# Kernel tuning notes

Measured on AMD Instinct MI355X. Metric: run time of the kernel, lower is better.

The kernel has to match this reference:

```python
import jax, jax.numpy as jnp
import numpy as np
import math

WIN = 7
PAD = WIN // 2
DOWN = 4
OCC_SCALE = 2.0
GROUPS = 8
GN_EPS = 1e-5
OCC_EPS = 1e-6


def group_norm(x, w, b):
    # x: [B, C, H, W]; normalize within channel groups (torch GroupNorm)
    B, C, H, W = x.shape
    xg = x.reshape(B, GROUPS, C // GROUPS, H, W)
    mu = xg.mean(axis=(2, 3, 4), keepdims=True)
    var = xg.var(axis=(2, 3, 4), keepdims=True)
    xn = ((xg - mu) * jax.lax.rsqrt(var + GN_EPS)).reshape(B, C, H, W)
    return xn * w[None, :, None, None] + b[None, :, None, None]


def avg_pool(x):
    s = jax.lax.reduce_window(x, 0.0, jax.lax.add, (1, 1, DOWN, DOWN), (1, 1, DOWN, DOWN), 'VALID')
    return s / (DOWN * DOWN)


def max_pool(x):
    return jax.lax.reduce_window(x, -jnp.inf, jax.lax.max, (1, 1, DOWN, DOWN), (1, 1, DOWN, DOWN), 'VALID')


def unfold(x):
    # kernel positions in row-major (i-major) order, matching torch layout.
    B, C, h, w = x.shape
    xp = jnp.pad(x, ((0, 0), (0, 0), (PAD, PAD), (PAD, PAD)))
    pats = jnp.stack([xp[:, :, i:i + h, j:j + w] for i in range(WIN) for j in range(WIN)], axis=2)
    return pats


def reference(img_bev, rad_bev, occ_prob, Wq, Wk, Wv, Wo, gq_w, gq_b, gk_w, gk_b, alpha):
    B, C, H, W = img_bev.shape
    img = avg_pool(img_bev)
    rad = max_pool(rad_bev)
    occ = max_pool(occ_prob)

    q = group_norm(jnp.einsum('oc,bchw->bohw', Wq, img), gq_w, gq_b)
    k = group_norm(jnp.einsum('oc,bchw->bohw', Wk, rad), gk_w, gk_b)
    v = jnp.einsum('oc,bchw->bohw', Wv, rad)

    _, d, h, w = q.shape
    HW = h * w
    P = WIN * WIN

    k_nb = unfold(k).reshape(B, d, P, HW).transpose(0, 3, 2, 1)  # [B,HW,P,d]
    v_nb = unfold(v).reshape(B, d, P, HW).transpose(0, 3, 2, 1)  # [B,HW,P,d]
    q_flat = q.reshape(B, d, HW).transpose(0, 2, 1)              # [B,HW,d]

    logits = jnp.einsum('bnd,bnpd->bnp', q_flat, k_nb) / math.sqrt(d)
    occ_nb = unfold(occ).reshape(B, P, HW).transpose(0, 2, 1)    # [B,HW,P]
    logits = logits + OCC_SCALE * jnp.log(jnp.clip(occ_nb, OCC_EPS, None))

    att = jax.nn.softmax(logits, axis=-1)
    msg = jnp.einsum('bnp,bnpd->bnd', att, v_nb)                 # [B,HW,d]
    msg = msg.transpose(0, 2, 1).reshape(B, d, h, w)
    msg = jnp.einsum('od,bdhw->bohw', Wo, msg)
    msg = msg * jnp.clip(occ, 0.0, 1.0)
    msg = jax.image.resize(msg, (B, C, H, W), method='bilinear')  # align_corners=False
    return img_bev + alpha * msg


def setup_inputs() -> dict:
    key = jax.random.key(0)
    ks = jax.random.split(key, 12)
    B, C_IMG, C_RAD, H, W, D = 2, 256, 128, 384, 384, 64
    inp = {
        'img_bev': jax.random.normal(ks[0], (B, C_IMG, H, W), jnp.float32),
        'rad_bev': jax.random.normal(ks[1], (B, C_RAD, H, W), jnp.float32),
        'occ_prob': jax.random.uniform(ks[2], (B, 1, H, W), jnp.float32),
        'Wq': jax.random.normal(ks[3], (D, C_IMG), jnp.float32) / np.sqrt(C_IMG),
        'Wk': jax.random.normal(ks[4], (D, C_RAD), jnp.float32) / np.sqrt(C_RAD),
        'Wv': jax.random.normal(ks[5], (D, C_RAD), jnp.float32) / np.sqrt(C_RAD),
        'Wo': jax.random.normal(ks[6], (C_IMG, D), jnp.float32) / np.sqrt(D),
        'gq_w': jnp.ones((D,), jnp.float32),
        'gq_b': jnp.zeros((D,), jnp.float32),
        'gk_w': jnp.ones((D,), jnp.float32),
        'gk_b': jnp.zeros((D,), jnp.float32),
        'alpha': jnp.float32(0.1),
    }
    return inp
```

## Files before the change

### kernel.cpp

```cpp
#include <hip/hip_runtime.h>
#include <math.h>


namespace {
constexpr int HIN  = 384;
constexpr int WIN_ = 384;
constexpr int HP   = 96;
constexpr int WPX  = 96;
constexpr int NP   = HP * WPX;
constexpr int CIMG = 256;
constexpr int CRAD = 128;
constexpr int DD   = 64;
constexpr int BB   = 2;
constexpr float OOB_LOGIT = -27.631021115928547f;

constexpr size_t OFF_IMGP = 0;
constexpr size_t OFF_RADP = OFF_IMGP + (size_t)BB * CIMG * NP;
constexpr size_t OFF_OCCP = OFF_RADP + (size_t)BB * CRAD * NP;
constexpr size_t OFF_OCCL = OFF_OCCP + (size_t)BB * NP;
constexpr size_t OFF_Q    = OFF_OCCL + (size_t)BB * NP;
constexpr size_t OFF_K    = OFF_Q + (size_t)BB * NP * DD;
constexpr size_t OFF_V    = OFF_K + (size_t)BB * NP * DD;
constexpr size_t OFF_MSG  = OFF_V + (size_t)BB * NP * DD;
constexpr size_t OFF_MSGO = OFF_MSG + (size_t)BB * NP * DD;
constexpr size_t OFF_WOT  = OFF_MSGO + (size_t)BB * CIMG * NP;
constexpr size_t OFF_STAT = OFF_WOT + (size_t)DD * CIMG;
constexpr size_t OFF_COEF = OFF_STAT + 64;
}

__global__ __launch_bounds__(256) void pool_kernel(const float* __restrict__ img,
                                                   const float* __restrict__ rad,
                                                   const float* __restrict__ occ,
                                                   float* __restrict__ ws) {
  int bid = blockIdx.x;
  int tid = threadIdx.x;
  const float* src;
  float* dst;
  float* occl = nullptr;
  int mode;
  if (bid < BB * CIMG) {
    src = img + (size_t)bid * HIN * WIN_;
    dst = ws + OFF_IMGP + (size_t)bid * NP;
    mode = 0;
  } else if (bid < BB * CIMG + BB * CRAD) {
    int r = bid - BB * CIMG;
    src = rad + (size_t)r * HIN * WIN_;
    dst = ws + OFF_RADP + (size_t)r * NP;
    mode = 1;
  } else {
    int r = bid - BB * CIMG - BB * CRAD;
    src = occ + (size_t)r * HIN * WIN_;
    dst = ws + OFF_OCCP + (size_t)r * NP;
    occl = ws + OFF_OCCL + (size_t)r * NP;
    mode = 2;
  }
  for (int it = 0; it < NP / 256; ++it) {
    int idx = it * 256 + tid;
    int oy = idx / WPX, ox = idx % WPX;
    const float* p = src + (size_t)(oy * 4) * WIN_ + ox * 4;
    if (mode == 0) {
      float s = 0.f;
#pragma unroll
      for (int r = 0; r < 4; ++r) {
        float4 v = *(const float4*)(p + (size_t)r * WIN_);
        s += v.x + v.y + v.z + v.w;
      }
      dst[idx] = s * 0.0625f;
    } else {
      float m = -INFINITY;
#pragma unroll
      for (int r = 0; r < 4; ++r) {
        float4 v = *(const float4*)(p + (size_t)r * WIN_);
        m = fmaxf(m, fmaxf(fmaxf(v.x, v.y), fmaxf(v.z, v.w)));
      }
      dst[idx] = m;
      if (mode == 2) occl[idx] = 2.0f * logf(fmaxf(m, 1e-6f));
    }
  }
}

__global__ __launch_bounds__(256) void proj_q_kernel(const float* __restrict__ Wq,
                                                     float* __restrict__ ws) {
  __shared__ float Xs[32 * 64];
  __shared__ float Wss[32 * 64];
  __shared__ float sstat[16];
  int bid = blockIdx.x;
  int b = bid / (NP / 64);
  int n0 = (bid % (NP / 64)) * 64;
  int tid = threadIdx.x;
  int og = tid & 15, ng = tid >> 4;
  if (tid < 16) sstat[tid] = 0.f;
  float4 acc[4];
#pragma unroll
  for (int j = 0; j < 4; ++j) acc[j] = make_float4(0.f, 0.f, 0.f, 0.f);
  const float* X = ws + OFF_IMGP + (size_t)b * CIMG * NP;
  for (int c0 = 0; c0 < CIMG; c0 += 32) {
    {
      int cc = tid >> 3, seg = tid & 7;
      const float* g = X + (size_t)(c0 + cc) * NP + n0 + seg * 8;
      float4 a0 = *(const float4*)g;
      float4 a1 = *(const float4*)(g + 4);
      *(float4*)&Xs[cc * 64 + seg * 8] = a0;
      *(float4*)&Xs[cc * 64 + seg * 8 + 4] = a1;
    }
    {
      int o = tid & 63, q8 = tid >> 6;
      const float* g = Wq + (size_t)o * CIMG + c0 + q8 * 8;
      float4 a0 = *(const float4*)g;
      float4 a1 = *(const float4*)(g + 4);
      Wss[(q8 * 8 + 0) * 64 + o] = a0.x;
      Wss[(q8 * 8 + 1) * 64 + o] = a0.y;
      Wss[(q8 * 8 + 2) * 64 + o] = a0.z;
      Wss[(q8 * 8 + 3) * 64 + o] = a0.w;
      Wss[(q8 * 8 + 4) * 64 + o] = a1.x;
      Wss[(q8 * 8 + 5) * 64 + o] = a1.y;
      Wss[(q8 * 8 + 6) * 64 + o] = a1.z;
      Wss[(q8 * 8 + 7) * 64 + o] = a1.w;
    }
    __syncthreads();
#pragma unroll
    for (int cc = 0; cc < 32; ++cc) {
      float4 wv = *(const float4*)&Wss[cc * 64 + og * 4];
      float4 xv = *(const float4*)&Xs[cc * 64 + ng * 4];
      acc[0].x = fmaf(wv.x, xv.x, acc[0].x); acc[0].y = fmaf(wv.y, xv.x, acc[0].y);
      acc[0].z = fmaf(wv.z, xv.x, acc[0].z); acc[0].w = fmaf(wv.w, xv.x, acc[0].w);
      acc[1].x = fmaf(wv.x, xv.y, acc[1].x); acc[1].y = fmaf(wv.y, xv.y, acc[1].y);
      acc[1].z = fmaf(wv.z, xv.y, acc[1].z); acc[1].w = fmaf(wv.w, xv.y, acc[1].w);
      acc[2].x = fmaf(wv.x, xv.z, acc[2].x); acc[2].y = fmaf(wv.y, xv.z, acc[2].y);
      acc[2].z = fmaf(wv.z, xv.z, acc[2].z); acc[2].w = fmaf(wv.w, xv.z, acc[2].w);
      acc[3].x = fmaf(wv.x, xv.w, acc[3].x); acc[3].y = fmaf(wv.y, xv.w, acc[3].y);
      acc[3].z = fmaf(wv.z, xv.w, acc[3].z); acc[3].w = fmaf(wv.w, xv.w, acc[3].w);
    }
    __syncthreads();
  }
  float* outq = ws + OFF_Q + (size_t)b * NP * DD;
#pragma unroll
  for (int j = 0; j < 4; ++j) {
    *(float4*)&outq[(size_t)(n0 + ng * 4 + j) * DD + og * 4] = acc[j];
  }
  float s1 = 0.f, s2 = 0.f;
#pragma unroll
  for (int j = 0; j < 4; ++j) {
    s1 += acc[j].x + acc[j].y + acc[j].z + acc[j].w;
    s2 += acc[j].x * acc[j].x + acc[j].y * acc[j].y + acc[j].z * acc[j].z + acc[j].w * acc[j].w;
  }
  int g = og >> 1;
  atomicAdd(&sstat[g * 2], s1);
  atomicAdd(&sstat[g * 2 + 1], s2);
  __syncthreads();
  if (tid < 16) atomicAdd(&ws[OFF_STAT + b * 16 + tid], sstat[tid]);
}

__global__ __launch_bounds__(256) void proj_kv_kernel(const float* __restrict__ Wk,
                                                      const float* __restrict__ Wv,
                                                      float* __restrict__ ws) {
  __shared__ float Xs[32 * 64];
  __shared__ float Wsk[32 * 64];
  __shared__ float Wsv[32 * 64];
  __shared__ float sstat[16];
  int bid = blockIdx.x;
  int b = bid / (NP / 64);
  int n0 = (bid % (NP / 64)) * 64;
  int tid = threadIdx.x;
  int og = tid & 15, ng = tid >> 4;
  if (tid < 16) sstat[tid] = 0.f;
  float4 acck[4], accv[4];
#pragma unroll
  for (int j = 0; j < 4; ++j) {
    acck[j] = make_float4(0.f, 0.f, 0.f, 0.f);
    accv[j] = make_float4(0.f, 0.f, 0.f, 0.f);
  }
  const float* X = ws + OFF_RADP + (size_t)b * CRAD * NP;
  for (int c0 = 0; c0 < CRAD; c0 += 32) {
    {
      int cc = tid >> 3, seg = tid & 7;
      const float* g = X + (size_t)(c0 + cc) * NP + n0 + seg * 8;
      float4 a0 = *(const float4*)g;
      float4 a1 = *(const float4*)(g + 4);
      *(float4*)&Xs[cc * 64 + seg * 8] = a0;
      *(float4*)&Xs[cc * 64 + seg * 8 + 4] = a1;
    }
    {
      int o = tid & 63, q8 = tid >> 6;
      const float* gk = Wk + (size_t)o * CRAD + c0 + q8 * 8;
      const float* gv = Wv + (size_t)o * CRAD + c0 + q8 * 8;
      float4 k0 = *(const float4*)gk;
      float4 k1 = *(const float4*)(gk + 4);
      float4 v0 = *(const float4*)gv;
      float4 v1 = *(const float4*)(gv + 4);
      Wsk[(q8 * 8 + 0) * 64 + o] = k0.x; Wsk[(q8 * 8 + 1) * 64 + o] = k0.y;
      Wsk[(q8 * 8 + 2) * 64 + o] = k0.z; Wsk[(q8 * 8 + 3) * 64 + o] = k0.w;
      Wsk[(q8 * 8 + 4) * 64 + o] = k1.x; Wsk[(q8 * 8 + 5) * 64 + o] = k1.y;
      Wsk[(q8 * 8 + 6) * 64 + o] = k1.z; Wsk[(q8 * 8 + 7) * 64 + o] = k1.w;
      Wsv[(q8 * 8 + 0) * 64 + o] = v0.x; Wsv[(q8 * 8 + 1) * 64 + o] = v0.y;
      Wsv[(q8 * 8 + 2) * 64 + o] = v0.z; Wsv[(q8 * 8 + 3) * 64 + o] = v0.w;
      Wsv[(q8 * 8 + 4) * 64 + o] = v1.x; Wsv[(q8 * 8 + 5) * 64 + o] = v1.y;
      Wsv[(q8 * 8 + 6) * 64 + o] = v1.z; Wsv[(q8 * 8 + 7) * 64 + o] = v1.w;
    }
    __syncthreads();
#pragma unroll
    for (int cc = 0; cc < 32; ++cc) {
      float4 wk = *(const float4*)&Wsk[cc * 64 + og * 4];
      float4 wv = *(const float4*)&Wsv[cc * 64 + og * 4];
      float4 xv = *(const float4*)&Xs[cc * 64 + ng * 4];
      float xs;
      xs = xv.x;
      acck[0].x = fmaf(wk.x, xs, acck[0].x); acck[0].y = fmaf(wk.y, xs, acck[0].y);
      acck[0].z = fmaf(wk.z, xs, acck[0].z); acck[0].w = fmaf(wk.w, xs, acck[0].w);
      accv[0].x = fmaf(wv.x, xs, accv[0].x); accv[0].y = fmaf(wv.y, xs, accv[0].y);
      accv[0].z = fmaf(wv.z, xs, accv[0].z); accv[0].w = fmaf(wv.w, xs, accv[0].w);
      xs = xv.y;
      acck[1].x = fmaf(wk.x, xs, acck[1].x); acck[1].y = fmaf(wk.y, xs, acck[1].y);
      acck[1].z = fmaf(wk.z, xs, acck[1].z); acck[1].w = fmaf(wk.w, xs, acck[1].w);
      accv[1].x = fmaf(wv.x, xs, accv[1].x); accv[1].y = fmaf(wv.y, xs, accv[1].y);
      accv[1].z = fmaf(wv.z, xs, accv[1].z); accv[1].w = fmaf(wv.w, xs, accv[1].w);
      xs = xv.z;
      acck[2].x = fmaf(wk.x, xs, acck[2].x); acck[2].y = fmaf(wk.y, xs, acck[2].y);
      acck[2].z = fmaf(wk.z, xs, acck[2].z); acck[2].w = fmaf(wk.w, xs, acck[2].w);
      accv[2].x = fmaf(wv.x, xs, accv[2].x); accv[2].y = fmaf(wv.y, xs, accv[2].y);
      accv[2].z = fmaf(wv.z, xs, accv[2].z); accv[2].w = fmaf(wv.w, xs, accv[2].w);
      xs = xv.w;
      acck[3].x = fmaf(wk.x, xs, acck[3].x); acck[3].y = fmaf(wk.y, xs, acck[3].y);
      acck[3].z = fmaf(wk.z, xs, acck[3].z); acck[3].w = fmaf(wk.w, xs, acck[3].w);
      accv[3].x = fmaf(wv.x, xs, accv[3].x); accv[3].y = fmaf(wv.y, xs, accv[3].y);
      accv[3].z = fmaf(wv.z, xs, accv[3].z); accv[3].w = fmaf(wv.w, xs, accv[3].w);
    }
    __syncthreads();
  }
  float* outk = ws + OFF_K + (size_t)b * NP * DD;
  float* outv = ws + OFF_V + (size_t)b * NP * DD;
#pragma unroll
  for (int j = 0; j < 4; ++j) {
    *(float4*)&outk[(size_t)(n0 + ng * 4 + j) * DD + og * 4] = acck[j];
    *(float4*)&outv[(size_t)(n0 + ng * 4 + j) * DD + og * 4] = accv[j];
  }
  float s1 = 0.f, s2 = 0.f;
#pragma unroll
  for (int j = 0; j < 4; ++j) {
    s1 += acck[j].x + acck[j].y + acck[j].z + acck[j].w;
    s2 += acck[j].x * acck[j].x + acck[j].y * acck[j].y + acck[j].z * acck[j].z +
          acck[j].w * acck[j].w;
  }
  int g = og >> 1;
  atomicAdd(&sstat[g * 2], s1);
  atomicAdd(&sstat[g * 2 + 1], s2);
  __syncthreads();
  if (tid < 16) atomicAdd(&ws[OFF_STAT + 32 + b * 16 + tid], sstat[tid]);
}

__global__ void coef_kernel(const float* __restrict__ gqw, const float* __restrict__ gqb,
                            const float* __restrict__ gkw, const float* __restrict__ gkb,
                            const float* __restrict__ Wo, float* __restrict__ ws) {
  int tid = threadIdx.x;
  const float Nf = 8.f * NP;
  float* stat = ws + OFF_STAT;
  float* coef = ws + OFF_COEF;
  if (tid < 128) {
    int b = tid >> 6, o = tid & 63, g = o >> 3;
    float s1 = stat[(b * 8 + g) * 2], s2 = stat[(b * 8 + g) * 2 + 1];
    float mu = s1 / Nf;
    float var = s2 / Nf - mu * mu;
    float rstd = rsqrtf(var + 1e-5f);
    coef[tid] = rstd * gqw[o];
    coef[128 + tid] = gqb[o] - mu * rstd * gqw[o];
    s1 = stat[32 + (b * 8 + g) * 2];
    s2 = stat[32 + (b * 8 + g) * 2 + 1];
    mu = s1 / Nf;
    var = s2 / Nf - mu * mu;
    rstd = rsqrtf(var + 1e-5f);
    coef[256 + tid] = rstd * gkw[o];
    coef[384 + tid] = gkb[o] - mu * rstd * gkw[o];
  }
  float* WoT = ws + OFF_WOT;
  for (int i = 0; i < 64; ++i) WoT[i * 256 + tid] = Wo[(size_t)tid * 64 + i];
}

__global__ __launch_bounds__(256) void attn_kernel(float* __restrict__ ws) {
  int tid = threadIdx.x;
  int lane = tid & 63, widx = tid >> 6;
  int pos = blockIdx.x * 4 + widx;
  int b = pos / NP, n = pos % NP;
  int y = n / WPX, x = n % WPX;
  const float* coef = ws + OFF_COEF;
  float aq = coef[b * 64 + lane], bq = coef[128 + b * 64 + lane];
  float ak = coef[256 + b * 64 + lane], bk = coef[384 + b * 64 + lane];
  const float* qb = ws + OFF_Q + (size_t)b * NP * DD;
  const float* kb = ws + OFF_K + (size_t)b * NP * DD;
  const float* vb = ws + OFF_V + (size_t)b * NP * DD;
  const float* occl = ws + OFF_OCCL + (size_t)b * NP;
  float qn = fmaf(qb[(size_t)n * DD + lane], aq, bq);
  float m = -1e30f, l = 0.f, acc = 0.f;
  for (int dy = -3; dy <= 3; ++dy) {
    int yy = y + dy;
    for (int dx = -3; dx <= 3; ++dx) {
      int xx = x + dx;
      bool in = ((unsigned)yy < (unsigned)HP) && ((unsigned)xx < (unsigned)WPX);
      float logit, vv;
      if (in) {
        int nb = yy * WPX + xx;
        float kn = fmaf(kb[(size_t)nb * DD + lane], ak, bk);
        float t = qn * kn;
        t += __shfl_xor(t, 1);
        t += __shfl_xor(t, 2);
        t += __shfl_xor(t, 4);
        t += __shfl_xor(t, 8);
        t += __shfl_xor(t, 16);
        t += __shfl_xor(t, 32);
        logit = fmaf(t, 0.125f, occl[nb]);
        vv = vb[(size_t)nb * DD + lane];
      } else {
        logit = OOB_LOGIT;
        vv = 0.f;
      }
      float mn = fmaxf(m, logit);
      float cor = __expf(m - mn);
      float wgt = __expf(logit - mn);
      l = fmaf(l, cor, wgt);
      acc = fmaf(acc, cor, wgt * vv);
      m = mn;
    }
  }
  ws[OFF_MSG + ((size_t)b * NP + n) * DD + lane] = acc / l;
}

__global__ __launch_bounds__(256) void wo_kernel(float* __restrict__ ws) {
  __shared__ float Ms[32 * 64];
  __shared__ float T[256 * 33];
  int bid = blockIdx.x;
  int b = bid / (NP / 32);
  int n0 = (bid % (NP / 32)) * 32;
  int tid = threadIdx.x;
  const float* msg = ws + OFF_MSG + ((size_t)b * NP + n0) * DD;
  {
    float4 a0 = *(const float4*)(msg + tid * 8);
    float4 a1 = *(const float4*)(msg + tid * 8 + 4);
    *(float4*)&Ms[tid * 8] = a0;
    *(float4*)&Ms[tid * 8 + 4] = a1;
  }
  __syncthreads();
  const float* WoT = ws + OFF_WOT;
  float acc[32];
#pragma unroll
  for (int n = 0; n < 32; ++n) acc[n] = 0.f;
  for (int dc = 0; dc < 64; dc += 16) {
    float w[16];
#pragma unroll
    for (int i = 0; i < 16; ++i) w[i] = WoT[(size_t)(dc + i) * 256 + tid];
#pragma unroll
    for (int n = 0; n < 32; ++n) {
      const float* mr = &Ms[n * 64 + dc];
      float s = acc[n];
#pragma unroll
      for (int i = 0; i < 16; ++i) s = fmaf(w[i], mr[i], s);
      acc[n] = s;
    }
  }
  const float* occp = ws + OFF_OCCP + (size_t)b * NP + n0;
#pragma unroll
  for (int n = 0; n < 32; ++n) {
    float oc = occp[n];
    oc = fminf(fmaxf(oc, 0.f), 1.f);
    T[tid * 33 + n] = acc[n] * oc;
  }
  __syncthreads();
  float* msgo = ws + OFF_MSGO + (size_t)b * CIMG * NP;
  for (int rep = 0; rep < 32; ++rep) {
    int idx = rep * 256 + tid;
    int c = idx >> 5, n = idx & 31;
    msgo[(size_t)c * NP + n0 + n] = T[c * 33 + n];
  }
}

__global__ __launch_bounds__(256) void final_kernel(const float* __restrict__ img,
                                                    const float* __restrict__ ws,
                                                    const float* __restrict__ alpha_p,
                                                    float* __restrict__ out) {
  size_t idx = (size_t)blockIdx.x * 256 + threadIdx.x;
  int xq = (int)(idx % 96);
  size_t t1 = idx / 96;
  int y = (int)(t1 % 384);
  size_t t2 = t1 / 384;
  int c = (int)(t2 % 256);
  int b = (int)(t2 / 256);
  float alpha = *alpha_p;
  const float* mrow = ws + OFF_MSGO + (size_t)(b * 256 + c) * NP;
  float sy = y * 0.25f - 0.375f;
  float jf = floorf(sy);
  float fy = sy - jf;
  int j0 = (int)jf;
  int j1 = j0 + 1;
  j0 = max(j0, 0);
  j1 = min(j1, HP - 1);
  int iL = max(xq - 1, 0), iC = xq, iR = min(xq + 1, WPX - 1);
  const float* r0 = mrow + (size_t)j0 * WPX;
  const float* r1 = mrow + (size_t)j1 * WPX;
  float cL = fmaf(fy, r1[iL] - r0[iL], r0[iL]);
  float cC = fmaf(fy, r1[iC] - r0[iC], r0[iC]);
  float cR = fmaf(fy, r1[iR] - r0[iR], r0[iR]);
  float4 v;
  v.x = fmaf(0.625f, cC - cL, cL);
  v.y = fmaf(0.875f, cC - cL, cL);
  v.z = fmaf(0.125f, cR - cC, cC);
  v.w = fmaf(0.375f, cR - cC, cC);
  size_t base = ((size_t)(b * 256 + c) * 384 + y) * 384 + (size_t)xq * 4;
  float4 im = *(const float4*)(img + base);
  float4 o;
  o.x = fmaf(alpha, v.x, im.x);
  o.y = fmaf(alpha, v.y, im.y);
  o.z = fmaf(alpha, v.z, im.z);
  o.w = fmaf(alpha, v.w, im.w);
  *(float4*)(out + base) = o;
}

extern "C" void kernel_launch(void* const* d_in, const int* in_sizes, int n_in,
                              void* d_out, int out_size, void* d_ws, size_t ws_size,
                              hipStream_t stream) {
  const float* img = (const float*)d_in[0];
  const float* rad = (const float*)d_in[1];
  const float* occ = (const float*)d_in[2];
  const float* Wq = (const float*)d_in[3];
  const float* Wk = (const float*)d_in[4];
  const float* Wv = (const float*)d_in[5];
  const float* Wo = (const float*)d_in[6];
  const float* gqw = (const float*)d_in[7];
  const float* gqb = (const float*)d_in[8];
  const float* gkw = (const float*)d_in[9];
  const float* gkb = (const float*)d_in[10];
  const float* alpha = (const float*)d_in[11];
  float* ws = (float*)d_ws;
  float* out = (float*)d_out;

  hipMemsetAsync(ws + OFF_STAT, 0, 64 * sizeof(float), stream);
  pool_kernel<<<BB * CIMG + BB * CRAD + BB, 256, 0, stream>>>(img, rad, occ, ws);
  proj_q_kernel<<<BB * (NP / 64), 256, 0, stream>>>(Wq, ws);
  proj_kv_kernel<<<BB * (NP / 64), 256, 0, stream>>>(Wk, Wv, ws);
  coef_kernel<<<1, 256, 0, stream>>>(gqw, gqb, gkw, gkb, Wo, ws);
  attn_kernel<<<BB * NP / 4, 256, 0, stream>>>(ws);
  wo_kernel<<<BB * (NP / 32), 256, 0, stream>>>(ws);
  final_kernel<<<(BB * 256 * 384 * 96) / 256, 256, 0, stream>>>(img, ws, alpha, out);
}
```

Measured before the change: 822.6 us.

## Merge Q and KV projection launches; pack four query positions per wavefront in attention

The two projection kernels are combined into one launch, with blocks split by index between the Q path and the K/V path. This lets both sets of work share the GPU at once and removes one launch boundary. The attention kernel now handles four query positions per 64-lane wavefront, with each lane owning four channels via float4 loads. That cuts the dot-product shuffle reduction from six steps to four and quarters the per-position exp/softmax bookkeeping. The cost is more registers per lane and a 16-lane reduction instead of a full-wave one.

```diff
diff --git a/kernel.cpp b/kernel.cpp
--- a/kernel.cpp
+++ b/kernel.cpp
@@ -79,173 +79,171 @@
   }
 }
 
-__global__ __launch_bounds__(256) void proj_q_kernel(const float* __restrict__ Wq,
-                                                     float* __restrict__ ws) {
-  __shared__ float Xs[32 * 64];
-  __shared__ float Wss[32 * 64];
-  __shared__ float sstat[16];
+__global__ __launch_bounds__(256) void proj_kernel(const float* __restrict__ Wq,
+                                                   const float* __restrict__ Wk,
+                                                   const float* __restrict__ Wv,
+                                                   float* __restrict__ ws) {
+  __shared__ float smem[3 * 32 * 64 + 16];
+  float* Xs = smem;
+  float* Wa = smem + 2048;
+  float* Wb = smem + 4096;
+  float* sstat = smem + 6144;
   int bid = blockIdx.x;
-  int b = bid / (NP / 64);
-  int n0 = (bid % (NP / 64)) * 64;
   int tid = threadIdx.x;
   int og = tid & 15, ng = tid >> 4;
   if (tid < 16) sstat[tid] = 0.f;
-  float4 acc[4];
-#pragma unroll
-  for (int j = 0; j < 4; ++j) acc[j] = make_float4(0.f, 0.f, 0.f, 0.f);
-  const float* X = ws + OFF_IMGP + (size_t)b * CIMG * NP;
-  for (int c0 = 0; c0 < CIMG; c0 += 32) {
-    {
-      int cc = tid >> 3, seg = tid & 7;
-      const float* g = X + (size_t)(c0 + cc) * NP + n0 + seg * 8;
-      float4 a0 = *(const float4*)g;
-      float4 a1 = *(const float4*)(g + 4);
-      *(float4*)&Xs[cc * 64 + seg * 8] = a0;
-      *(float4*)&Xs[cc * 64 + seg * 8 + 4] = a1;
-    }
-    {
-      int o = tid & 63, q8 = tid >> 6;
-      const float* g = Wq + (size_t)o * CIMG + c0 + q8 * 8;
-      float4 a0 = *(const float4*)g;
-      float4 a1 = *(const float4*)(g + 4);
-      Wss[(q8 * 8 + 0) * 64 + o] = a0.x;
-      Wss[(q8 * 8 + 1) * 64 + o] = a0.y;
-      Wss[(q8 * 8 + 2) * 64 + o] = a0.z;
-      Wss[(q8 * 8 + 3) * 64 + o] = a0.w;
-      Wss[(q8 * 8 + 4) * 64 + o] = a1.x;
-      Wss[(q8 * 8 + 5) * 64 + o] = a1.y;
-      Wss[(q8 * 8 + 6) * 64 + o] = a1.z;
-      Wss[(q8 * 8 + 7) * 64 + o] = a1.w;
-    }
+  const int NBLK = BB * (NP / 64);
+
+  if (bid < NBLK) {
+    int b = bid / (NP / 64);
+    int n0 = (bid % (NP / 64)) * 64;
+    float4 acc[4];
+#pragma unroll
+    for (int j = 0; j < 4; ++j) acc[j] = make_float4(0.f, 0.f, 0.f, 0.f);
+    const float* X = ws + OFF_IMGP + (size_t)b * CIMG * NP;
+    for (int c0 = 0; c0 < CIMG; c0 += 32) {
+      {
+        int cc = tid >> 3, seg = tid & 7;
+        const float* g = X + (size_t)(c0 + cc) * NP + n0 + seg * 8;
+        float4 a0 = *(const float4*)g;
+        float4 a1 = *(const float4*)(g + 4);
+        *(float4*)&Xs[cc * 64 + seg * 8] = a0;
+        *(float4*)&Xs[cc * 64 + seg * 8 + 4] = a1;
+      }
+      {
+        int o = tid & 63, q8 = tid >> 6;
+        const float* g = Wq + (size_t)o * CIMG + c0 + q8 * 8;
+        float4 a0 = *(const float4*)g;
+        float4 a1 = *(const float4*)(g + 4);
+        Wa[(q8 * 8 + 0) * 64 + o] = a0.x;
+        Wa[(q8 * 8 + 1) * 64 + o] = a0.y;
+        Wa[(q8 * 8 + 2) * 64 + o] = a0.z;
+        Wa[(q8 * 8 + 3) * 64 + o] = a0.w;
+        Wa[(q8 * 8 + 4) * 64 + o] = a1.x;
+        Wa[(q8 * 8 + 5) * 64 + o] = a1.y;
+        Wa[(q8 * 8 + 6) * 64 + o] = a1.z;
+        Wa[(q8 * 8 + 7) * 64 + o] = a1.w;
+      }
+      __syncthreads();
+#pragma unroll
+      for (int cc = 0; cc < 32; ++cc) {
+        float4 wv = *(const float4*)&Wa[cc * 64 + og * 4];
+        float4 xv = *(const float4*)&Xs[cc * 64 + ng * 4];
+        acc[0].x = fmaf(wv.x, xv.x, acc[0].x); acc[0].y = fmaf(wv.y, xv.x, acc[0].y);
+        acc[0].z = fmaf(wv.z, xv.x, acc[0].z); acc[0].w = fmaf(wv.w, xv.x, acc[0].w);
+        acc[1].x = fmaf(wv.x, xv.y, acc[1].x); acc[1].y = fmaf(wv.y, xv.y, acc[1].y);
+        acc[1].z = fmaf(wv.z, xv.y, acc[1].z); acc[1].w = fmaf(wv.w, xv.y, acc[1].w);
+        acc[2].x = fmaf(wv.x, xv.z, acc[2].x); acc[2].y = fmaf(wv.y, xv.z, acc[2].y);
+        acc[2].z = fmaf(wv.z, xv.z, acc[2].z); acc[2].w = fmaf(wv.w, xv.z, acc[2].w);
+        acc[3].x = fmaf(wv.x, xv.w, acc[3].x); acc[3].y = fmaf(wv.y, xv.w, acc[3].y);
+        acc[3].z = fmaf(wv.z, xv.w, acc[3].z); acc[3].w = fmaf(wv.w, xv.w, acc[3].w);
+      }
+      __syncthreads();
+    }
+    float* outq = ws + OFF_Q + (size_t)b * NP * DD;
+#pragma unroll
+    for (int j = 0; j < 4; ++j) {
+      *(float4*)&outq[(size_t)(n0 + ng * 4 + j) * DD + og * 4] = acc[j];
+    }
+    float s1 = 0.f, s2 = 0.f;
+#pragma unroll
+    for (int j = 0; j < 4; ++j) {
+      s1 += acc[j].x + acc[j].y + acc[j].z + acc[j].w;
+      s2 += acc[j].x * acc[j].x + acc[j].y * acc[j].y + acc[j].z * acc[j].z +
+            acc[j].w * acc[j].w;
+    }
+    int g = og >> 1;
+    atomicAdd(&sstat[g * 2], s1);
+    atomicAdd(&sstat[g * 2 + 1], s2);
     __syncthreads();
-#pragma unroll
-    for (int cc = 0; cc < 32; ++cc) {
-      float4 wv = *(const float4*)&Wss[cc * 64 + og * 4];
-      float4 xv = *(const float4*)&Xs[cc * 64 + ng * 4];
-      acc[0].x = fmaf(wv.x, xv.x, acc[0].x); acc[0].y = fmaf(wv.y, xv.x, acc[0].y);
-      acc[0].z = fmaf(wv.z, xv.x, acc[0].z); acc[0].w = fmaf(wv.w, xv.x, acc[0].w);
-      acc[1].x = fmaf(wv.x, xv.y, acc[1].x); acc[1].y = fmaf(wv.y, xv.y, acc[1].y);
-      acc[1].z = fmaf(wv.z, xv.y, acc[1].z); acc[1].w = fmaf(wv.w, xv.y, acc[1].w);
-      acc[2].x = fmaf(wv.x, xv.z, acc[2].x); acc[2].y = fmaf(wv.y, xv.z, acc[2].y);
-      acc[2].z = fmaf(wv.z, xv.z, acc[2].z); acc[2].w = fmaf(wv.w, xv.z, acc[2].w);
-      acc[3].x = fmaf(wv.x, xv.w, acc[3].x); acc[3].y = fmaf(wv.y, xv.w, acc[3].y);
-      acc[3].z = fmaf(wv.z, xv.w, acc[3].z); acc[3].w = fmaf(wv.w, xv.w, acc[3].w);
-    }
+    if (tid < 16) atomicAdd(&ws[OFF_STAT + b * 16 + tid], sstat[tid]);
+  } else {
+    int r = bid - NBLK;
+    int b = r / (NP / 64);
+    int n0 = (r % (NP / 64)) * 64;
+    float4 acck[4], accv[4];
+#pragma unroll
+    for (int j = 0; j < 4; ++j) {
+      acck[j] = make_float4(0.f, 0.f, 0.f, 0.f);
+      accv[j] = make_float4(0.f, 0.f, 0.f, 0.f);
+    }
+    const float* X = ws + OFF_RADP + (size_t)b * CRAD * NP;
+    for (int c0 = 0; c0 < CRAD; c0 += 32) {
+      {
+        int cc = tid >> 3, seg = tid & 7;
+        const float* g = X + (size_t)(c0 + cc) * NP + n0 + seg * 8;
+        float4 a0 = *(const float4*)g;
+        float4 a1 = *(const float4*)(g + 4);
+        *(float4*)&Xs[cc * 64 + seg * 8] = a0;
+        *(float4*)&Xs[cc * 64 + seg * 8 + 4] = a1;
+      }
+      {
+        int o = tid & 63, q8 = tid >> 6;
+        const float* gk = Wk + (size_t)o * CRAD + c0 + q8 * 8;
+        const float* gv = Wv + (size_t)o * CRAD + c0 + q8 * 8;
+        float4 k0 = *(const float4*)gk;
+        float4 k1 = *(const float4*)(gk + 4);
+        float4 v0 = *(const float4*)gv;
+        float4 v1 = *(const float4*)(gv + 4);
+        Wa[(q8 * 8 + 0) * 64 + o] = k0.x; Wa[(q8 * 8 + 1) * 64 + o] = k0.y;
+        Wa[(q8 * 8 + 2) * 64 + o] = k0.z; Wa[(q8 * 8 + 3) * 64 + o] = k0.w;
+        Wa[(q8 * 8 + 4) * 64 + o] = k1.x; Wa[(q8 * 8 + 5) * 64 + o] = k1.y;
+        Wa[(q8 * 8 + 6) * 64 + o] = k1.z; Wa[(q8 * 8 + 7) * 64 + o] = k1.w;
+        Wb[(q8 * 8 + 0) * 64 + o] = v0.x; Wb[(q8 * 8 + 1) * 64 + o] = v0.y;
+        Wb[(q8 * 8 + 2) * 64 + o] = v0.z; Wb[(q8 * 8 + 3) * 64 + o] = v0.w;
+        Wb[(q8 * 8 + 4) * 64 + o] = v1.x; Wb[(q8 * 8 + 5) * 64 + o] = v1.y;
+        Wb[(q8 * 8 + 6) * 64 + o] = v1.z; Wb[(q8 * 8 + 7) * 64 + o] = v1.w;
+      }
+      __syncthreads();
+#pragma unroll
+      for (int cc = 0; cc < 32; ++cc) {
+        float4 wk = *(const float4*)&Wa[cc * 64 + og * 4];
+        float4 wv = *(const float4*)&Wb[cc * 64 + og * 4];
+        float4 xv = *(const float4*)&Xs[cc * 64 + ng * 4];
+        float xs;
+        xs = xv.x;
+        acck[0].x = fmaf(wk.x, xs, acck[0].x); acck[0].y = fmaf(wk.y, xs, acck[0].y);
+        acck[0].z = fmaf(wk.z, xs, acck[0].z); acck[0].w = fmaf(wk.w, xs, acck[0].w);
+        accv[0].x = fmaf(wv.x, xs, accv[0].x); accv[0].y = fmaf(wv.y, xs, accv[0].y);
+        accv[0].z = fmaf(wv.z, xs, accv[0].z); accv[0].w = fmaf(wv.w, xs, accv[0].w);
+        xs = xv.y;
+        acck[1].x = fmaf(wk.x, xs, acck[1].x); acck[1].y = fmaf(wk.y, xs, acck[1].y);
+        acck[1].z = fmaf(wk.z, xs, acck[1].z); acck[1].w = fmaf(wk.w, xs, acck[1].w);
+        accv[1].x = fmaf(wv.x, xs, accv[1].x); accv[1].y = fmaf(wv.y, xs, accv[1].y);
+        accv[1].z = fmaf(wv.z, xs, accv[1].z); accv[1].w = fmaf(wv.w, xs, accv[1].w);
+        xs = xv.z;
+        acck[2].x = fmaf(wk.x, xs, acck[2].x); acck[2].y = fmaf(wk.y, xs, acck[2].y);
+        acck[2].z = fmaf(wk.z, xs, acck[2].z); acck[2].w = fmaf(wk.w, xs, acck[2].w);
+        accv[2].x = fmaf(wv.x, xs, accv[2].x); accv[2].y = fmaf(wv.y, xs, accv[2].y);
+        accv[2].z = fmaf(wv.z, xs, accv[2].z); accv[2].w = fmaf(wv.w, xs, accv[2].w);
+        xs = xv.w;
+        acck[3].x = fmaf(wk.x, xs, acck[3].x); acck[3].y = fmaf(wk.y, xs, acck[3].y);
+        acck[3].z = fmaf(wk.z, xs, acck[3].z); acck[3].w = fmaf(wk.w, xs, acck[3].w);
+        accv[3].x = fmaf(wv.x, xs, accv[3].x); accv[3].y = fmaf(wv.y, xs, accv[3].y);
+        accv[3].z = fmaf(wv.z, xs, accv[3].z); accv[3].w = fmaf(wv.w, xs, accv[3].w);
+      }
+      __syncthreads();
+    }
+    float* outk = ws + OFF_K + (size_t)b * NP * DD;
+    float* outv = ws + OFF_V + (size_t)b * NP * DD;
+#pragma unroll
+    for (int j = 0; j < 4; ++j) {
+      *(float4*)&outk[(size_t)(n0 + ng * 4 + j) * DD + og * 4] = acck[j];
+      *(float4*)&outv[(size_t)(n0 + ng * 4 + j) * DD + og * 4] = accv[j];
+    }
+    float s1 = 0.f, s2 = 0.f;
+#pragma unroll
+    for (int j = 0; j < 4; ++j) {
+      s1 += acck[j].x + acck[j].y + acck[j].z + acck[j].w;
+      s2 += acck[j].x * acck[j].x + acck[j].y * acck[j].y + acck[j].z * acck[j].z +
+            acck[j].w * acck[j].w;
+    }
+    int g = og >> 1;
+    atomicAdd(&sstat[g * 2], s1);
+    atomicAdd(&sstat[g * 2 + 1], s2);
     __syncthreads();
-  }
-  float* outq = ws + OFF_Q + (size_t)b * NP * DD;
-#pragma unroll
-  for (int j = 0; j < 4; ++j) {
-    *(float4*)&outq[(size_t)(n0 + ng * 4 + j) * DD + og * 4] = acc[j];
-  }
-  float s1 = 0.f, s2 = 0.f;
-#pragma unroll
-  for (int j = 0; j < 4; ++j) {
-    s1 += acc[j].x + acc[j].y + acc[j].z + acc[j].w;
-    s2 += acc[j].x * acc[j].x + acc[j].y * acc[j].y + acc[j].z * acc[j].z + acc[j].w * acc[j].w;
-  }
-  int g = og >> 1;
-  atomicAdd(&sstat[g * 2], s1);
-  atomicAdd(&sstat[g * 2 + 1], s2);
-  __syncthreads();
-  if (tid < 16) atomicAdd(&ws[OFF_STAT + b * 16 + tid], sstat[tid]);
-}
-
-__global__ __launch_bounds__(256) void proj_kv_kernel(const float* __restrict__ Wk,
-                                                      const float* __restrict__ Wv,
-                                                      float* __restrict__ ws) {
-  __shared__ float Xs[32 * 64];
-  __shared__ float Wsk[32 * 64];
-  __shared__ float Wsv[32 * 64];
-  __shared__ float sstat[16];
-  int bid = blockIdx.x;
-  int b = bid / (NP / 64);
-  int n0 = (bid % (NP / 64)) * 64;
-  int tid = threadIdx.x;
-  int og = tid & 15, ng = tid >> 4;
-  if (tid < 16) sstat[tid] = 0.f;
-  float4 acck[4], accv[4];
-#pragma unroll
-  for (int j = 0; j < 4; ++j) {
-    acck[j] = make_float4(0.f, 0.f, 0.f, 0.f);
-    accv[j] = make_float4(0.f, 0.f, 0.f, 0.f);
-  }
-  const float* X = ws + OFF_RADP + (size_t)b * CRAD * NP;
-  for (int c0 = 0; c0 < CRAD; c0 += 32) {
-    {
-      int cc = tid >> 3, seg = tid & 7;
-      const float* g = X + (size_t)(c0 + cc) * NP + n0 + seg * 8;
-      float4 a0 = *(const float4*)g;
-      float4 a1 = *(const float4*)(g + 4);
-      *(float4*)&Xs[cc * 64 + seg * 8] = a0;
-      *(float4*)&Xs[cc * 64 + seg * 8 + 4] = a1;
-    }
-    {
-      int o = tid & 63, q8 = tid >> 6;
-      const float* gk = Wk + (size_t)o * CRAD + c0 + q8 * 8;
-      const float* gv = Wv + (size_t)o * CRAD + c0 + q8 * 8;
-      float4 k0 = *(const float4*)gk;
-      float4 k1 = *(const float4*)(gk + 4);
-      float4 v0 = *(const float4*)gv;
-      float4 v1 = *(const float4*)(gv + 4);
-      Wsk[(q8 * 8 + 0) * 64 + o] = k0.x; Wsk[(q8 * 8 + 1) * 64 + o] = k0.y;
-      Wsk[(q8 * 8 + 2) * 64 + o] = k0.z; Wsk[(q8 * 8 + 3) * 64 + o] = k0.w;
-      Wsk[(q8 * 8 + 4) * 64 + o] = k1.x; Wsk[(q8 * 8 + 5) * 64 + o] = k1.y;
-      Wsk[(q8 * 8 + 6) * 64 + o] = k1.z; Wsk[(q8 * 8 + 7) * 64 + o] = k1.w;
-      Wsv[(q8 * 8 + 0) * 64 + o] = v0.x; Wsv[(q8 * 8 + 1) * 64 + o] = v0.y;
-      Wsv[(q8 * 8 + 2) * 64 + o] = v0.z; Wsv[(q8 * 8 + 3) * 64 + o] = v0.w;
-      Wsv[(q8 * 8 + 4) * 64 + o] = v1.x; Wsv[(q8 * 8 + 5) * 64 + o] = v1.y;
-      Wsv[(q8 * 8 + 6) * 64 + o] = v1.z; Wsv[(q8 * 8 + 7) * 64 + o] = v1.w;
-    }
-    __syncthreads();
-#pragma unroll
-    for (int cc = 0; cc < 32; ++cc) {
-      float4 wk = *(const float4*)&Wsk[cc * 64 + og * 4];
-      float4 wv = *(const float4*)&Wsv[cc * 64 + og * 4];
-      float4 xv = *(const float4*)&Xs[cc * 64 + ng * 4];
-      float xs;
-      xs = xv.x;
-      acck[0].x = fmaf(wk.x, xs, acck[0].x); acck[0].y = fmaf(wk.y, xs, acck[0].y);
-      acck[0].z = fmaf(wk.z, xs, acck[0].z); acck[0].w = fmaf(wk.w, xs, acck[0].w);
-      accv[0].x = fmaf(wv.x, xs, accv[0].x); accv[0].y = fmaf(wv.y, xs, accv[0].y);
-      accv[0].z = fmaf(wv.z, xs, accv[0].z); accv[0].w = fmaf(wv.w, xs, accv[0].w);
-      xs = xv.y;
-      acck[1].x = fmaf(wk.x, xs, acck[1].x); acck[1].y = fmaf(wk.y, xs, acck[1].y);
-      acck[1].z = fmaf(wk.z, xs, acck[1].z); acck[1].w = fmaf(wk.w, xs, acck[1].w);
-      accv[1].x = fmaf(wv.x, xs, accv[1].x); accv[1].y = fmaf(wv.y, xs, accv[1].y);
-      accv[1].z = fmaf(wv.z, xs, accv[1].z); accv[1].w = fmaf(wv.w, xs, accv[1].w);
-      xs = xv.z;
-      acck[2].x = fmaf(wk.x, xs, acck[2].x); acck[2].y = fmaf(wk.y, xs, acck[2].y);
-      acck[2].z = fmaf(wk.z, xs, acck[2].z); acck[2].w = fmaf(wk.w, xs, acck[2].w);
-      accv[2].x = fmaf(wv.x, xs, accv[2].x); accv[2].y = fmaf(wv.y, xs, accv[2].y);
-      accv[2].z = fmaf(wv.z, xs, accv[2].z); accv[2].w = fmaf(wv.w, xs, accv[2].w);
-      xs = xv.w;
-      acck[3].x = fmaf(wk.x, xs, acck[3].x); acck[3].y = fmaf(wk.y, xs, acck[3].y);
-      acck[3].z = fmaf(wk.z, xs, acck[3].z); acck[3].w = fmaf(wk.w, xs, acck[3].w);
-      accv[3].x = fmaf(wv.x, xs, accv[3].x); accv[3].y = fmaf(wv.y, xs, accv[3].y);
-      accv[3].z = fmaf(wv.z, xs, accv[3].z); accv[3].w = fmaf(wv.w, xs, accv[3].w);
-    }
-    __syncthreads();
-  }
-  float* outk = ws + OFF_K + (size_t)b * NP * DD;
-  float* outv = ws + OFF_V + (size_t)b * NP * DD;
-#pragma unroll
-  for (int j = 0; j < 4; ++j) {
-    *(float4*)&outk[(size_t)(n0 + ng * 4 + j) * DD + og * 4] = acck[j];
-    *(float4*)&outv[(size_t)(n0 + ng * 4 + j) * DD + og * 4] = accv[j];
-  }
-  float s1 = 0.f, s2 = 0.f;
-#pragma unroll
-  for (int j = 0; j < 4; ++j) {
-    s1 += acck[j].x + acck[j].y + acck[j].z + acck[j].w;
-    s2 += acck[j].x * acck[j].x + acck[j].y * acck[j].y + acck[j].z * acck[j].z +
-          acck[j].w * acck[j].w;
-  }
-  int g = og >> 1;
-  atomicAdd(&sstat[g * 2], s1);
-  atomicAdd(&sstat[g * 2 + 1], s2);
-  __syncthreads();
-  if (tid < 16) atomicAdd(&ws[OFF_STAT + 32 + b * 16 + tid], sstat[tid]);
+    if (tid < 16) atomicAdd(&ws[OFF_STAT + 32 + b * 16 + tid], sstat[tid]);
+  }
 }
 
 __global__ void coef_kernel(const float* __restrict__ gqw, const float* __restrict__ gqb,
@@ -278,49 +276,73 @@
 __global__ __launch_bounds__(256) void attn_kernel(float* __restrict__ ws) {
   int tid = threadIdx.x;
   int lane = tid & 63, widx = tid >> 6;
-  int pos = blockIdx.x * 4 + widx;
+  int grp = lane >> 4;
+  int sl = lane & 15;
+  int d0 = sl * 4;
+  int pos = blockIdx.x * 16 + widx * 4 + grp;
   int b = pos / NP, n = pos % NP;
   int y = n / WPX, x = n % WPX;
   const float* coef = ws + OFF_COEF;
-  float aq = coef[b * 64 + lane], bq = coef[128 + b * 64 + lane];
-  float ak = coef[256 + b * 64 + lane], bk = coef[384 + b * 64 + lane];
+  float4 aq = *(const float4*)&coef[b * 64 + d0];
+  float4 bq = *(const float4*)&coef[128 + b * 64 + d0];
+  float4 ak = *(const float4*)&coef[256 + b * 64 + d0];
+  float4 bk = *(const float4*)&coef[384 + b * 64 + d0];
   const float* qb = ws + OFF_Q + (size_t)b * NP * DD;
   const float* kb = ws + OFF_K + (size_t)b * NP * DD;
   const float* vb = ws + OFF_V + (size_t)b * NP * DD;
   const float* occl = ws + OFF_OCCL + (size_t)b * NP;
-  float qn = fmaf(qb[(size_t)n * DD + lane], aq, bq);
-  float m = -1e30f, l = 0.f, acc = 0.f;
+  float4 qv = *(const float4*)&qb[(size_t)n * DD + d0];
+  float4 qn;
+  qn.x = fmaf(qv.x, aq.x, bq.x);
+  qn.y = fmaf(qv.y, aq.y, bq.y);
+  qn.z = fmaf(qv.z, aq.z, bq.z);
+  qn.w = fmaf(qv.w, aq.w, bq.w);
+  float m = -1e30f, l = 0.f;
+  float4 acc = make_float4(0.f, 0.f, 0.f, 0.f);
   for (int dy = -3; dy <= 3; ++dy) {
     int yy = y + dy;
+    bool rowin = (unsigned)yy < (unsigned)HP;
     for (int dx = -3; dx <= 3; ++dx) {
       int xx = x + dx;
-      bool in = ((unsigned)yy < (unsigned)HP) && ((unsigned)xx < (unsigned)WPX);
-      float logit, vv;
+      bool in = rowin && ((unsigned)xx < (unsigned)WPX);
+      float logit;
+      float4 vv;
       if (in) {
         int nb = yy * WPX + xx;
-        float kn = fmaf(kb[(size_t)nb * DD + lane], ak, bk);
-        float t = qn * kn;
+        float4 kv = *(const float4*)&kb[(size_t)nb * DD + d0];
+        vv = *(const float4*)&vb[(size_t)nb * DD + d0];
+        float t;
+        t = qn.x * fmaf(kv.x, ak.x, bk.x);
+        t = fmaf(qn.y, fmaf(kv.y, ak.y, bk.y), t);
+        t = fmaf(qn.z, fmaf(kv.z, ak.z, bk.z), t);
+        t = fmaf(qn.w, fmaf(kv.w, ak.w, bk.w), t);
         t += __shfl_xor(t, 1);
         t += __shfl_xor(t, 2);
         t += __shfl_xor(t, 4);
         t += __shfl_xor(t, 8);
-        t += __shfl_xor(t, 16);
-        t += __shfl_xor(t, 32);
         logit = fmaf(t, 0.125f, occl[nb]);
-        vv = vb[(size_t)nb * DD + lane];
       } else {
         logit = OOB_LOGIT;
-        vv = 0.f;
+        vv = make_float4(0.f, 0.f, 0.f, 0.f);
       }
       float mn = fmaxf(m, logit);
       float cor = __expf(m - mn);
       float wgt = __expf(logit - mn);
       l = fmaf(l, cor, wgt);
-      acc = fmaf(acc, cor, wgt * vv);
+      acc.x = fmaf(acc.x, cor, wgt * vv.x);
+      acc.y = fmaf(acc.y, cor, wgt * vv.y);
+      acc.z = fmaf(acc.z, cor, wgt * vv.z);
+      acc.w = fmaf(acc.w, cor, wgt * vv.w);
       m = mn;
     }
   }
-  ws[OFF_MSG + ((size_t)b * NP + n) * DD + lane] = acc / l;
+  float rl = 1.0f / l;
+  float4 o;
+  o.x = acc.x * rl;
+  o.y = acc.y * rl;
+  o.z = acc.z * rl;
+  o.w = acc.w * rl;
+  *(float4*)&ws[OFF_MSG + ((size_t)b * NP + n) * DD + d0] = o;
 }
 
 __global__ __launch_bounds__(256) void wo_kernel(float* __restrict__ ws) {
@@ -432,10 +454,9 @@
 
   hipMemsetAsync(ws + OFF_STAT, 0, 64 * sizeof(float), stream);
   pool_kernel<<<BB * CIMG + BB * CRAD + BB, 256, 0, stream>>>(img, rad, occ, ws);
-  proj_q_kernel<<<BB * (NP / 64), 256, 0, stream>>>(Wq, ws);
-  proj_kv_kernel<<<BB * (NP / 64), 256, 0, stream>>>(Wk, Wv, ws);
+  proj_kernel<<<2 * BB * (NP / 64), 256, 0, stream>>>(Wq, Wk, Wv, ws);
   coef_kernel<<<1, 256, 0, stream>>>(gqw, gqb, gkw, gkb, Wo, ws);
-  attn_kernel<<<BB * NP / 4, 256, 0, stream>>>(ws);
+  attn_kernel<<<BB * NP / 16, 256, 0, stream>>>(ws);
   wo_kernel<<<BB * (NP / 32), 256, 0, stream>>>(ws);
   final_kernel<<<(BB * 256 * 384 * 96) / 256, 256, 0, stream>>>(img, ws, alpha, out);
 }
```

Measured after the change: 766.6 us. 6.8% less time.
